# Performance work log

Hardware: AMD Instinct MI355X
Metric: run time of the kernel (lower is better)

## Reference

```python
import itertools
import jax, jax.numpy as jnp
import numpy as np


def setup_inputs() -> dict:
    key = jax.random.key(0)
    k1, k2 = jax.random.split(key)
    B, X, Y, Z, C = 2, 160, 192, 160, 1
    vol = jax.random.normal(k1, (B, X, Y, Z, C), dtype=jnp.float32)
    trf = jax.random.normal(k2, (B, X, Y, Z, 3), dtype=jnp.float32)  # dense displacement field
    return {"vol": vol, "trf": trf}


def _warp(vol, trf):
    # vol: [B, *spatial, C]; trf: [B, *spatial, nd] displacement (indexing='ij')
    B = vol.shape[0]
    spatial = vol.shape[1:-1]
    nd = len(spatial)
    C = vol.shape[-1]
    N = int(np.prod(spatial))

    grids = jnp.meshgrid(*[jnp.arange(s, dtype=jnp.float32) for s in spatial], indexing="ij")
    # absolute sample locations per dim: [B, *spatial]
    loc = [grids[d][None] + trf[..., d] for d in range(nd)]

    max_loc = [s - 1 for s in spatial]
    loc0 = [jnp.clip(jnp.floor(loc[d]), 0.0, max_loc[d]) for d in range(nd)]
    loc1 = [jnp.clip(loc0[d] + 1.0, 0.0, max_loc[d]) for d in range(nd)]
    clipped = [jnp.clip(loc[d], 0.0, max_loc[d]) for d in range(nd)]
    # neurite weight convention: weight for corner bit 0 is (loc1 - loc), for bit 1 is (1 - that)
    w1 = [loc1[d] - clipped[d] for d in range(nd)]   # weight when corner uses loc0
    w0 = [1.0 - w1[d] for d in range(nd)]            # weight when corner uses loc1
    i0 = [loc0[d].astype(jnp.int32) for d in range(nd)]
    i1 = [loc1[d].astype(jnp.int32) for d in range(nd)]

    vol_flat = vol.reshape(B, N, C)

    out = jnp.zeros((B,) + spatial + (C,), dtype=vol.dtype)
    for corner in itertools.product([0, 1], repeat=nd):
        subs = [(i1[d] if corner[d] else i0[d]) for d in range(nd)]
        ind = subs[0]
        for d in range(1, nd):
            ind = ind * spatial[d] + subs[d]  # row-major sub2ind
        vals = jnp.take_along_axis(vol_flat, ind.reshape(B, N)[..., None], axis=1)
        vals = vals.reshape((B,) + spatial + (C,))
        wt = (w0[0] if corner[0] else w1[0])
        for d in range(1, nd):
            wt = wt * (w0[d] if corner[d] else w1[d])
        out = out + wt[..., None] * vals
    return out


def reference(vol, trf):
    # indexing='ij', single_transform=False, fill_value=None (clamp to edge), linear interp.
    # The layer also passes trf through unchanged; we return the warped volume.
    return _warp(vol, trf)
```

## Files before the change

kernel.cpp:

```cpp
#include <hip/hip_runtime.h>

constexpr int B = 2, X = 160, Y = 192, Z = 160;
constexpr int TXs = 8, TYs = 8, TZs = 16;
constexpr int XT = X / TXs, YT = Y / TYs, ZT = Z / TZs;
constexpr int NTILES = B * XT * YT * ZT;
constexpr int NXCD = 8;
constexpr int CHUNK = NTILES / NXCD;
constexpr int RX = 16, RY = 16, RZ = 24;
constexpr int PLANE = RX * RY + 1;
constexpr int LDSF = RZ * PLANE;

typedef float f32x4 __attribute__((ext_vector_type(4)));

__global__ __launch_bounds__(256, 6) void warp_kernel(
    const float* __restrict__ vol,
    const float* __restrict__ trf,
    float* __restrict__ out)
{
    __shared__ float lds[LDSF];

    const int tid = threadIdx.x;
    const int bid = blockIdx.x;

    const int eff = (bid & (NXCD - 1)) * CHUNK + (bid >> 3);

    int tz = eff % ZT;
    int r  = eff / ZT;
    int ty = r % YT;
    int r2 = r / YT;
    int tx = r2 % XT;
    int b  = r2 / XT;

    const int xs = tx * TXs - 4;
    const int ys = ty * TYs - 4;
    const int zs = tz * TZs - 4;
    const int bX = b * X;

    {
        int row = (tid * 171) >> 10;
        int j   = tid - 6 * row;
#pragma unroll
        for (int k = 0; k < 6; ++k) {
            int xi = row >> 4;
            int yi = row & 15;
            int xg = min(max(xs + xi, 0), X - 1);
            int yg = min(max(ys + yi, 0), Y - 1);
            int zg = min(max(zs + 4 * j, 0), Z - 4);
            const f32x4 v = *reinterpret_cast<const f32x4*>(
                vol + ((size_t)(bX + xg) * Y + yg) * Z + zg);
            int w0 = 1028 * j + row;
            lds[w0]             = v.x;
            lds[w0 + PLANE]     = v.y;
            lds[w0 + 2 * PLANE] = v.z;
            lds[w0 + 3 * PLANE] = v.w;
            int jn = j + 4;
            bool wrap = (jn >= 6);
            j   = wrap ? jn - 6 : jn;
            row += wrap ? 43 : 42;
        }
    }
    __syncthreads();

    int zq = tid & 3;
    int ly = (tid >> 2) & 7;
    int lx = tid >> 5;
    int x  = tx * TXs + lx;
    int y  = ty * TYs + ly;
    int z0v = tz * TZs + 4 * zq;

    size_t vid0 = ((size_t)(bX + x) * Y + y) * Z + z0v;

    const f32x4* tp = reinterpret_cast<const f32x4*>(trf + vid0 * 3);
    f32x4 t0 = tp[0], t1 = tp[1], t2 = tp[2];
    float d[12] = {t0.x, t0.y, t0.z, t0.w,
                   t1.x, t1.y, t1.z, t1.w,
                   t2.x, t2.y, t2.z, t2.w};

    const float mx = (float)(X - 1), my = (float)(Y - 1), mz = (float)(Z - 1);
    const float fxc = (float)x, fyc = (float)y;

    float res[4];
#pragma unroll
    for (int e = 0; e < 4; ++e) {
        float lxf = fxc + d[3 * e + 0];
        float lyf = fyc + d[3 * e + 1];
        float lzf = (float)(z0v + e) + d[3 * e + 2];

        float clx = fminf(fmaxf(lxf, 0.0f), mx);
        float flx = floorf(clx);
        float fx  = clx - flx;
        int   ix0 = (int)flx;

        float cly = fminf(fmaxf(lyf, 0.0f), my);
        float fly = floorf(cly);
        float fy  = cly - fly;
        int   iy0 = (int)fly;

        float clz = fminf(fmaxf(lzf, 0.0f), mz);
        float flz = floorf(clz);
        float fz  = clz - flz;
        int   iz0 = (int)flz;

        int ux0 = ix0 - xs, uy0 = iy0 - ys, uz0 = iz0 - zs;

        bool ok = ((unsigned)ux0 < (unsigned)(RX - 1)) &
                  ((unsigned)uy0 < (unsigned)(RY - 1)) &
                  ((unsigned)uz0 < (unsigned)(RZ - 1));

        float v000, v001, v010, v011, v100, v101, v110, v111;
        if (ok) {
            int w = uz0 * PLANE + (ux0 << 4) + uy0;
            v000 = lds[w];
            v001 = lds[w + PLANE];
            v010 = lds[w + 1];
            v011 = lds[w + PLANE + 1];
            v100 = lds[w + 16];
            v101 = lds[w + PLANE + 16];
            v110 = lds[w + 17];
            v111 = lds[w + PLANE + 17];
        } else {
            int ix1 = min(ix0 + 1, X - 1);
            int iy1 = min(iy0 + 1, Y - 1);
            int iz1 = min(iz0 + 1, Z - 1);
            size_t g00 = ((size_t)(bX + ix0) * Y + iy0) * Z;
            size_t g01 = ((size_t)(bX + ix0) * Y + iy1) * Z;
            size_t g10 = ((size_t)(bX + ix1) * Y + iy0) * Z;
            size_t g11 = ((size_t)(bX + ix1) * Y + iy1) * Z;
            v000 = vol[g00 + iz0];
            v001 = vol[g00 + iz1];
            v010 = vol[g01 + iz0];
            v011 = vol[g01 + iz1];
            v100 = vol[g10 + iz0];
            v101 = vol[g10 + iz1];
            v110 = vol[g11 + iz0];
            v111 = vol[g11 + iz1];
        }

        float c00 = v000 + fz * (v001 - v000);
        float c01 = v010 + fz * (v011 - v010);
        float c10 = v100 + fz * (v101 - v100);
        float c11 = v110 + fz * (v111 - v110);
        float c0  = c00 + fy * (c01 - c00);
        float c1  = c10 + fy * (c11 - c10);
        res[e] = c0 + fx * (c1 - c0);
    }

    f32x4 o;
    o.x = res[0]; o.y = res[1]; o.z = res[2]; o.w = res[3];
    *reinterpret_cast<f32x4*>(out + vid0) = o;
}

extern "C" void kernel_launch(void* const* d_in, const int* in_sizes, int n_in,
                              void* d_out, int out_size, void* d_ws, size_t ws_size,
                              hipStream_t stream) {
    const float* vol = (const float*)d_in[0];
    const float* trf = (const float*)d_in[1];
    float* out = (float*)d_out;

    warp_kernel<<<NTILES, 256, 0, stream>>>(vol, trf, out);
}
```

Baseline: 44.71 us.

## Switch LDS halo to z-contiguous rows and fetch corner pairs with 2-wide loads

Changes the shared-memory halo layout from z-planes to z-contiguous rows padded to stride 27. Each trilinear corner pair along z can then be read with one 8-byte load, so four LDS reads replace eight. The halo shrinks to 15 x-rows, and the fill loop becomes a guarded linear chunk loop. Risks include unaligned 2-wide LDS accesses, possible bank conflicts at stride 27, and a smaller halo that sends more samples to the global fallback path.

```diff
diff --git a/kernel.cpp b/kernel.cpp
--- a/kernel.cpp
+++ b/kernel.cpp
@@ -6,11 +6,14 @@
 constexpr int NTILES = B * XT * YT * ZT;
 constexpr int NXCD = 8;
 constexpr int CHUNK = NTILES / NXCD;
-constexpr int RX = 16, RY = 16, RZ = 24;
-constexpr int PLANE = RX * RY + 1;
-constexpr int LDSF = RZ * PLANE;
+constexpr int RX = 15, RY = 16, RZ = 24;
+constexpr int RSTRIDE = 27;
+constexpr int NROWS = RX * RY;
+constexpr int LDSF = NROWS * RSTRIDE;
+constexpr int NCHUNKS = NROWS * 6;
 
 typedef float f32x4 __attribute__((ext_vector_type(4)));
+typedef float f32x2a __attribute__((ext_vector_type(2), aligned(4)));
 
 __global__ __launch_bounds__(256, 6) void warp_kernel(
     const float* __restrict__ vol,
@@ -37,26 +40,25 @@
     const int bX = b * X;
 
     {
-        int row = (tid * 171) >> 10;
-        int j   = tid - 6 * row;
 #pragma unroll
         for (int k = 0; k < 6; ++k) {
-            int xi = row >> 4;
-            int yi = row & 15;
-            int xg = min(max(xs + xi, 0), X - 1);
-            int yg = min(max(ys + yi, 0), Y - 1);
-            int zg = min(max(zs + 4 * j, 0), Z - 4);
-            const f32x4 v = *reinterpret_cast<const f32x4*>(
-                vol + ((size_t)(bX + xg) * Y + yg) * Z + zg);
-            int w0 = 1028 * j + row;
-            lds[w0]             = v.x;
-            lds[w0 + PLANE]     = v.y;
-            lds[w0 + 2 * PLANE] = v.z;
-            lds[w0 + 3 * PLANE] = v.w;
-            int jn = j + 4;
-            bool wrap = (jn >= 6);
-            j   = wrap ? jn - 6 : jn;
-            row += wrap ? 43 : 42;
+            unsigned c = (unsigned)tid + k * 256u;
+            if (c < (unsigned)NCHUNKS) {
+                unsigned row = c / 6u;
+                unsigned j   = c - 6u * row;
+                int xi  = (int)(row >> 4);
+                int yi  = (int)(row & 15u);
+                int xg  = min(max(xs + xi, 0), X - 1);
+                int yg  = min(max(ys + yi, 0), Y - 1);
+                int zg  = min(max(zs + 4 * (int)j, 0), Z - 4);
+                const f32x4 v = *reinterpret_cast<const f32x4*>(
+                    vol + ((size_t)(bX + xg) * Y + yg) * Z + zg);
+                int a = (int)row * RSTRIDE + 4 * (int)j;
+                lds[a + 0] = v.x;
+                lds[a + 1] = v.y;
+                lds[a + 2] = v.z;
+                lds[a + 3] = v.w;
+            }
         }
     }
     __syncthreads();
@@ -109,15 +111,15 @@
 
         float v000, v001, v010, v011, v100, v101, v110, v111;
         if (ok) {
-            int w = uz0 * PLANE + (ux0 << 4) + uy0;
-            v000 = lds[w];
-            v001 = lds[w + PLANE];
-            v010 = lds[w + 1];
-            v011 = lds[w + PLANE + 1];
-            v100 = lds[w + 16];
-            v101 = lds[w + PLANE + 16];
-            v110 = lds[w + 17];
-            v111 = lds[w + PLANE + 17];
+            int w = ((ux0 << 4) + uy0) * RSTRIDE + uz0;
+            f32x2a p00 = *reinterpret_cast<const f32x2a*>(&lds[w]);
+            f32x2a p01 = *reinterpret_cast<const f32x2a*>(&lds[w + RSTRIDE]);
+            f32x2a p10 = *reinterpret_cast<const f32x2a*>(&lds[w + 16 * RSTRIDE]);
+            f32x2a p11 = *reinterpret_cast<const f32x2a*>(&lds[w + 17 * RSTRIDE]);
+            v000 = p00.x; v001 = p00.y;
+            v010 = p01.x; v011 = p01.y;
+            v100 = p10.x; v101 = p10.y;
+            v110 = p11.x; v111 = p11.y;
         } else {
             int ix1 = min(ix0 + 1, X - 1);
             int iy1 = min(iy0 + 1, Y - 1);
```

Result: faster. 41.70 us (-6.7%).
